# Performance work log

Hardware: AMD Instinct MI355X
Metric: run time of the kernel (lower is better)

Reference implementation:

```python
import jax, jax.numpy as jnp
import numpy as np

B, N, D = 1, 1024, 3584
H, KVH, HD = 28, 4, 128
I = 18944
SEC = [16, 24, 24]  # mrope_section, sums to HD//2
EPS_RMS = 1e-6
EPS_SM = 1e-6


def setup_inputs() -> dict:
    key = jax.random.key(0)
    ks = jax.random.split(key, 16)
    s = 0.02
    return {
        "hidden_states": jax.random.normal(ks[0], (B, N, D), jnp.float32),
        "cos": jax.random.uniform(ks[1], (3, B, N, HD), jnp.float32, -1.0, 1.0),
        "sin": jax.random.uniform(ks[2], (3, B, N, HD), jnp.float32, -1.0, 1.0),
        "prune_mask": jax.random.randint(ks[3], (B, N), 0, 2, jnp.int32),
        "Wq": jax.random.normal(ks[4], (D, H * HD), jnp.float32) * s,
        "bq": jnp.zeros((H * HD,), jnp.float32),
        "Wk": jax.random.normal(ks[5], (D, KVH * HD), jnp.float32) * s,
        "bk": jnp.zeros((KVH * HD,), jnp.float32),
        "Wv": jax.random.normal(ks[6], (D, KVH * HD), jnp.float32) * s,
        "bv": jnp.zeros((KVH * HD,), jnp.float32),
        "Wo": jax.random.normal(ks[7], (H * HD, D), jnp.float32) * s,
        "ln1_w": jnp.ones((D,), jnp.float32),
        "ln2_w": jnp.ones((D,), jnp.float32),
        "Wg": jax.random.normal(ks[8], (D, I), jnp.float32) * s,
        "Wu": jax.random.normal(ks[9], (D, I), jnp.float32) * s,
        "Wd": jax.random.normal(ks[10], (I, D), jnp.float32) * s,
    }


def _rmsnorm(x, w):
    v = jnp.mean(x * x, axis=-1, keepdims=True)
    return x * jax.lax.rsqrt(v + EPS_RMS) * w


def _rotate_half(x):
    h = x.shape[-1] // 2
    return jnp.concatenate([-x[..., h:], x[..., :h]], axis=-1)


def _mrope_select(t):
    # t: (3, B, N, HD) -> (B, 1, N, HD), picking section i from axis i%3
    parts, idx = [], 0
    for i, s in enumerate(SEC * 2):
        parts.append(t[i % 3, :, :, idx:idx + s])
        idx += s
    return jnp.concatenate(parts, axis=-1)[:, None]


def reference(hidden_states, cos, sin, prune_mask, Wq, bq, Wk, bk, Wv, bv, Wo,
              ln1_w, ln2_w, Wg, Wu, Wd):
    x = _rmsnorm(hidden_states, ln1_w)
    q = (x @ Wq + bq).reshape(B, N, H, HD).transpose(0, 2, 1, 3)
    k = (x @ Wk + bk).reshape(B, N, KVH, HD).transpose(0, 2, 1, 3)
    v = (x @ Wv + bv).reshape(B, N, KVH, HD).transpose(0, 2, 1, 3)

    cf, sf = _mrope_select(cos), _mrope_select(sin)
    q = q * cf + _rotate_half(q) * sf
    k = k * cf + _rotate_half(k) * sf

    groups = H // KVH
    k = jnp.repeat(k, groups, axis=1)  # (B,H,N,HD)
    v = jnp.repeat(v, groups, axis=1)

    scores = jnp.einsum("bhqd,bhkd->bhqk", q, k) / np.sqrt(HD).astype(np.float32)
    causal = jnp.tril(jnp.ones((N, N), bool))
    scores = jnp.where(causal, scores, jnp.float32(-1e9))

    # custom prune-masked softmax (softmax_with_mask)
    am = prune_mask.astype(jnp.float32)[:, None, None, :]  # (B,1,1,N)
    eye = jnp.eye(N, dtype=jnp.float32)
    am = am + (1.0 - am) * eye
    mx = jnp.max(scores, axis=-1, keepdims=True)
    e = jnp.exp(scores - mx) * am
    attn = (e + EPS_SM / N) / (jnp.sum(e, axis=-1, keepdims=True) + EPS_SM)

    o = jnp.einsum("bhqk,bhkd->bhqd", attn, v)
    o = o.transpose(0, 2, 1, 3).reshape(B, N, H * HD) @ Wo

    h = hidden_states + o
    y = _rmsnorm(h, ln2_w)
    mlp = (jax.nn.silu(y @ Wg) * (y @ Wu)) @ Wd
    return h + mlp
```

## Files before the change

kernel.cpp:

```cpp
#include <hip/hip_runtime.h>
#include <hip/hip_bf16.h>


#define SEQ   1024
#define DIM   3584
#define NH    28
#define NKVH  4
#define HDIM  128
#define IDIM  18944
#define QKVN  4608
#define GUN   37888

typedef __attribute__((ext_vector_type(8))) __bf16 bf16x8;
typedef __attribute__((ext_vector_type(4))) __bf16 bf16x4;
typedef __attribute__((ext_vector_type(4))) float  f32x4;

static constexpr size_t OFF_WQKVT = 0;
static constexpr size_t OFF_WOT   = OFF_WQKVT + (size_t)QKVN*DIM*2;
static constexpr size_t OFF_WGUT  = OFF_WOT   + (size_t)DIM*DIM*2;
static constexpr size_t OFF_WDT   = OFF_WGUT  + (size_t)GUN*DIM*2;
static constexpr size_t OFF_XB    = OFF_WDT   + (size_t)DIM*IDIM*2;
static constexpr size_t OFF_QKV   = OFF_XB    + (size_t)SEQ*DIM*2;
static constexpr size_t OFF_VT    = OFF_QKV   + (size_t)SEQ*QKVN*2;
static constexpr size_t OFF_VSUMP = OFF_VT    + (size_t)NKVH*HDIM*SEQ*2;
static constexpr size_t OFF_VSUM  = OFF_VSUMP + 4*8*128*4;
static constexpr size_t OFF_BQKV  = OFF_VSUM  + 4*128*4;
static constexpr size_t OFF_OB    = OFF_BQKV  + (size_t)QKVN*4;
static constexpr size_t OFF_HB    = OFF_OB    + (size_t)SEQ*DIM*2;
static constexpr size_t OFF_YB    = OFF_HB    + (size_t)SEQ*DIM*4;
static constexpr size_t OFF_GU    = OFF_YB    + (size_t)SEQ*DIM*2;
static constexpr size_t OFF_PB    = OFF_GU    + (size_t)SEQ*GUN*2;
static constexpr size_t OFF_PART  = OFF_GU;

#define GLL16(gp, lp)                                                        \
  __builtin_amdgcn_global_load_lds(                                         \
      (const __attribute__((address_space(1))) void*)(gp),                  \
      (__attribute__((address_space(3))) void*)(lp), 16, 0, 0)

#define BAR    asm volatile("s_barrier" ::: "memory")
#define LGKM0  asm volatile("s_waitcnt lgkmcnt(0)" ::: "memory")
#define VM4    asm volatile("s_waitcnt vmcnt(4)" ::: "memory")

__global__ __launch_bounds__(256) void transconv_kernel(
    const float* __restrict__ W, __bf16* __restrict__ WT, int K, int N, int mode)
{
  __shared__ __bf16 t[64][72];
  const int tid = threadIdx.x;
  const int k0 = blockIdx.y * 64, n0 = blockIdx.x * 64;
#pragma unroll
  for (int it = 0; it < 4; ++it) {
    int idx = it * 256 + tid;
    int r = idx >> 4, c4 = idx & 15;
    float4 v = *(const float4*)(W + (size_t)(k0 + r) * N + n0 + c4 * 4);
    t[r][c4 * 4 + 0] = (__bf16)v.x;
    t[r][c4 * 4 + 1] = (__bf16)v.y;
    t[r][c4 * 4 + 2] = (__bf16)v.z;
    t[r][c4 * 4 + 3] = (__bf16)v.w;
  }
  __syncthreads();
#pragma unroll
  for (int it = 0; it < 2; ++it) {
    int idx = it * 256 + tid;
    int r = idx >> 3, c8 = idx & 7;
    bf16x8 o;
#pragma unroll
    for (int i = 0; i < 8; ++i) o[i] = t[c8 * 8 + i][r];
    const int nlog = n0 + r;
    const int orow = (mode == 0) ? nlog
                   : ((nlog >> 4) << 5) + ((mode == 2) ? 16 : 0) + (nlog & 15);
    *(bf16x8*)(WT + (size_t)orow * K + k0 + c8 * 8) = o;
  }
}

__global__ __launch_bounds__(256) void pack_bias_kernel(
    const float* __restrict__ bq, const float* __restrict__ bk,
    const float* __restrict__ bv, float* __restrict__ out)
{
  int i = blockIdx.x * 256 + threadIdx.x;
  if (i < DIM) out[i] = bq[i];
  else if (i < DIM + 512) out[i] = bk[i - DIM];
  else if (i < QKVN) out[i] = bv[i - DIM - 512];
}

__global__ __launch_bounds__(256) void rmsnorm_kernel(
    const float* __restrict__ in, const float* __restrict__ w,
    __bf16* __restrict__ out)
{
  const int row = blockIdx.x;
  const int t = threadIdx.x;
  const float* x = in + (size_t)row * DIM;
  float4 v[4];
  float ss = 0.f;
#pragma unroll
  for (int i = 0; i < 4; ++i) {
    int idx = t + i * 256;
    if (idx < 896) {
      v[i] = ((const float4*)x)[idx];
      ss += v[i].x * v[i].x + v[i].y * v[i].y + v[i].z * v[i].z + v[i].w * v[i].w;
    }
  }
#pragma unroll
  for (int m = 1; m < 64; m <<= 1) ss += __shfl_xor(ss, m);
  __shared__ float red[4];
  if ((t & 63) == 0) red[t >> 6] = ss;
  __syncthreads();
  float tot = red[0] + red[1] + red[2] + red[3];
  float rs = rsqrtf(tot / (float)DIM + 1e-6f);
#pragma unroll
  for (int i = 0; i < 4; ++i) {
    int idx = t + i * 256;
    if (idx < 896) {
      float4 wv = ((const float4*)w)[idx];
      bf16x4 o;
      o[0] = (__bf16)(v[i].x * rs * wv.x);
      o[1] = (__bf16)(v[i].y * rs * wv.y);
      o[2] = (__bf16)(v[i].z * rs * wv.z);
      o[3] = (__bf16)(v[i].w * rs * wv.w);
      *(bf16x4*)(out + (size_t)row * DIM + idx * 4) = o;
    }
  }
}

template<int S, bool BF16OUT, bool BIAS>
__global__ __launch_bounds__(256) void reduce_kernel(
    const float* __restrict__ part, const float* __restrict__ resid,
    const float* __restrict__ bias, void* __restrict__ out, int N, int MN4)
{
  const int i4 = blockIdx.x * 256 + threadIdx.x;
  if (i4 >= MN4) return;
  const size_t base = (size_t)i4 * 4;
  f32x4 s = *(const f32x4*)(part + base);
#pragma unroll
  for (int k = 1; k < S; ++k)
    s += *(const f32x4*)(part + (size_t)k * MN4 * 4 + base);
  if (BIAS) {
    const int col = (int)(base % N);
    s += *(const f32x4*)(bias + col);
  }
  if (resid != nullptr) s += *(const f32x4*)(resid + base);
  if (BF16OUT) {
    bf16x4 o;
#pragma unroll
    for (int j = 0; j < 4; ++j) o[j] = (__bf16)s[j];
    *(bf16x4*)((__bf16*)out + base) = o;
  } else {
    *(f32x4*)((float*)out + base) = s;
  }
}

__global__ __launch_bounds__(256) void qkv_reduce_rope_kernel(
    const float* __restrict__ part, const float* __restrict__ bias,
    const float* __restrict__ cosb, const float* __restrict__ sinb,
    __bf16* __restrict__ qkv)
{
  const int n = blockIdx.x;
  const int t = threadIdx.x;
  const size_t rb = (size_t)n * QKVN;
  const size_t slab = (size_t)SEQ * QKVN;

  const int head = t >> 3;
  const int d0 = (t & 7) * 8;
  const int col = (head < NH) ? head * HDIM + d0 : DIM + (head - NH) * HDIM + d0;

  float lo[8], hi[8];
#pragma unroll
  for (int j = 0; j < 8; j += 4) {
    f32x4 a  = *(const f32x4*)(part + rb + col + j);
    f32x4 b  = *(const f32x4*)(part + slab + rb + col + j);
    f32x4 bi = *(const f32x4*)(bias + col + j);
    f32x4 a2  = *(const f32x4*)(part + rb + col + 64 + j);
    f32x4 b2  = *(const f32x4*)(part + slab + rb + col + 64 + j);
    f32x4 bi2 = *(const f32x4*)(bias + col + 64 + j);
#pragma unroll
    for (int i = 0; i < 4; ++i) {
      lo[j + i] = a[i] + b[i] + bi[i];
      hi[j + i] = a2[i] + b2[i] + bi2[i];
    }
  }
  bf16x8 olo, ohi;
#pragma unroll
  for (int j = 0; j < 8; ++j) {
    const int d = d0 + j;
    const int src = (d < 16) ? 0 : (d < 40) ? 1 : 2;
    const float* cb = cosb + ((size_t)src * SEQ + n) * HDIM;
    const float* sb = sinb + ((size_t)src * SEQ + n) * HDIM;
    const float c0 = cb[d], s0 = sb[d];
    const float c1 = cb[d + 64], s1 = sb[d + 64];
    olo[j] = (__bf16)(lo[j] * c0 - hi[j] * s0);
    ohi[j] = (__bf16)(hi[j] * c1 + lo[j] * s1);
  }
  *(bf16x8*)(qkv + rb + col) = olo;
  *(bf16x8*)(qkv + rb + col + 64) = ohi;

  {
    const int vc = 4096 + t * 2;
    float2 a  = *(const float2*)(part + rb + vc);
    float2 b  = *(const float2*)(part + slab + rb + vc);
    float2 bi = *(const float2*)(bias + vc);
    qkv[rb + vc]     = (__bf16)(a.x + b.x + bi.x);
    qkv[rb + vc + 1] = (__bf16)(a.y + b.y + bi.y);
  }
}

__global__ __launch_bounds__(256) void reduce_rms_kernel(
    const float* __restrict__ part, const float* __restrict__ resid,
    const float* __restrict__ w, float* __restrict__ hout,
    __bf16* __restrict__ yout)
{
  const int row = blockIdx.x;
  const int t = threadIdx.x;
  const size_t base = (size_t)row * DIM;
  const size_t slab = (size_t)SEQ * DIM;
  f32x4 v[4];
  float ss = 0.f;
#pragma unroll
  for (int i = 0; i < 4; ++i) {
    int idx = t + i * 256;
    if (idx < 896) {
      f32x4 s = *(const f32x4*)(part + base + idx * 4);
      s += *(const f32x4*)(part + slab + base + idx * 4);
      s += *(const f32x4*)(part + 2 * slab + base + idx * 4);
      s += *(const f32x4*)(part + 3 * slab + base + idx * 4);
      s += *(const f32x4*)(resid + base + idx * 4);
      v[i] = s;
      ss += s[0] * s[0] + s[1] * s[1] + s[2] * s[2] + s[3] * s[3];
      *(f32x4*)(hout + base + idx * 4) = s;
    }
  }
#pragma unroll
  for (int m = 1; m < 64; m <<= 1) ss += __shfl_xor(ss, m);
  __shared__ float red[4];
  if ((t & 63) == 0) red[t >> 6] = ss;
  __syncthreads();
  float tot = red[0] + red[1] + red[2] + red[3];
  float rs = rsqrtf(tot / (float)DIM + 1e-6f);
#pragma unroll
  for (int i = 0; i < 4; ++i) {
    int idx = t + i * 256;
    if (idx < 896) {
      f32x4 wv = *(const f32x4*)(w + idx * 4);
      bf16x4 o;
#pragma unroll
      for (int j = 0; j < 4; ++j) o[j] = (__bf16)(v[i][j] * rs * wv[j]);
      *(bf16x4*)(yout + base + idx * 4) = o;
    }
  }
}

template<int EPI>
__global__ __launch_bounds__(512, 1) void gemm256_kernel(
    const __bf16* __restrict__ A, const __bf16* __restrict__ BT,
    void* __restrict__ OUT, int M, int N, int K, int Kc, int gridY)
{
  __shared__ int4 lds4[8192];
  char* ldsc = (char*)lds4;
  const int tid = threadIdx.x;
  const int l = tid & 63, w = tid >> 6;
  const int wr = w >> 2, wc = w & 3;
  const int lg = l >> 4, lc = l & 15;

  const int nwg = gridDim.x;
  const int bq8 = nwg >> 3, br8 = nwg & 7;
  const int xcd = blockIdx.x & 7, bidx = blockIdx.x >> 3;
  const int wg = (xcd < br8 ? xcd * (bq8 + 1) : br8 * (bq8 + 1) + (xcd - br8) * bq8) + bidx;
  const int ntn = N >> 8;
  const int wg2 = wg / gridY;
  const int row0 = (wg % gridY) * 256;
  const int col0 = (wg2 % ntn) * 256;
  const int ks_ = wg2 / ntn;
  const int kbase = ks_ * Kc;

  size_t aoffj[2], boffj[2];
  int dstj[2];
#pragma unroll
  for (int j = 0; j < 2; ++j) {
    const int c = (j * 8 + w) * 64 + l;
    const int r = c >> 3, p = c & 7;
    const int b = p ^ (r & 7);
    aoffj[j] = (size_t)(row0 + r) * K + kbase + b * 8;
    boffj[j] = (size_t)(col0 + r) * K + kbase + b * 8;
    dstj[j] = (j * 8 + w) * 1024;
  }

#define STG_A(U, KT, BUFB) do {                                              \
    GLL16(A + aoffj[0] + (size_t)(U) * 128 * K + (size_t)(KT) * 64,          \
          ldsc + (BUFB) + (U) * 16384 + dstj[0]);                            \
    GLL16(A + aoffj[1] + (size_t)(U) * 128 * K + (size_t)(KT) * 64,          \
          ldsc + (BUFB) + (U) * 16384 + dstj[1]); } while (0)
#define STG_B(U, KT, BUFB) do {                                              \
    GLL16(BT + boffj[0] + (size_t)(U) * 128 * K + (size_t)(KT) * 64,         \
          ldsc + (BUFB) + 32768 + (U) * 16384 + dstj[0]);                    \
    GLL16(BT + boffj[1] + (size_t)(U) * 128 * K + (size_t)(KT) * 64,         \
          ldsc + (BUFB) + 32768 + (U) * 16384 + dstj[1]); } while (0)

  const int sw = lc & 7;
  const int rdA = (wr * 128 + lc) * 128;
  const int rdB = 32768 + (wc * 64 + lc) * 128;
  const int sk0 = (lg ^ sw) * 16;
  const int sk1 = ((4 | lg) ^ sw) * 16;

  f32x4 acc[8][4] = {};
  bf16x8 af[4][2], bfr[4][2];

#define RD_A4(MH, BUFB) do { _Pragma("unroll")                               \
    for (int mm = 0; mm < 4; ++mm) {                                         \
      af[mm][0] = *(const bf16x8*)(ldsc + (BUFB) + rdA + ((MH) * 4 + mm) * 2048 + sk0); \
      af[mm][1] = *(const bf16x8*)(ldsc + (BUFB) + rdA + ((MH) * 4 + mm) * 2048 + sk1); } } while (0)
#define RD_B2(NL, BUFB) do { _Pragma("unroll")                               \
    for (int nn = 0; nn < 2; ++nn) {                                         \
      bfr[(NL) + nn][0] = *(const bf16x8*)(ldsc + (BUFB) + rdB + ((NL) + nn) * 2048 + sk0); \
      bfr[(NL) + nn][1] = *(const bf16x8*)(ldsc + (BUFB) + rdB + ((NL) + nn) * 2048 + sk1); } } while (0)

#define MFMA16(MH, NL) do { _Pragma("unroll")                                \
    for (int mm = 0; mm < 4; ++mm) { _Pragma("unroll")                       \
      for (int nn = 0; nn < 2; ++nn) {                                       \
        acc[(MH)*4+mm][(NL)+nn] = __builtin_amdgcn_mfma_f32_16x16x32_bf16(   \
            af[mm][0], bfr[(NL)+nn][0], acc[(MH)*4+mm][(NL)+nn], 0, 0, 0);   \
        acc[(MH)*4+mm][(NL)+nn] = __builtin_amdgcn_mfma_f32_16x16x32_bf16(   \
            af[mm][1], bfr[(NL)+nn][1], acc[(MH)*4+mm][(NL)+nn], 0, 0, 0); } } } while (0)

#define DO_MFMA(MH, NL)                                                      \
    __builtin_amdgcn_s_setprio(1); MFMA16(MH, NL);                           \
    __builtin_amdgcn_s_setprio(0)

  STG_B(0, 0, 0); STG_B(1, 0, 0); STG_A(0, 0, 0); STG_A(1, 0, 0);
  STG_B(0, 1, 65536); STG_B(1, 1, 65536);
  VM4;
  BAR;
  RD_A4(0, 0); RD_B2(0, 0);

  const int T = Kc >> 6;
#pragma unroll 1
  for (int i = 0; i < (T >> 1); ++i) {
    const int t1 = 2 * i + 1;
    const int se = (2 * i + 2 < T) ? 2 * i + 2 : 2 * i;
    const int so = (2 * i + 3 < T) ? 2 * i + 3 : t1;
    LGKM0; DO_MFMA(0, 0); RD_B2(2, 0); STG_A(0, t1, 65536); BAR;
    LGKM0; DO_MFMA(0, 2); RD_A4(1, 0); STG_A(1, t1, 65536); BAR;
    LGKM0; DO_MFMA(1, 2); STG_B(0, se, 0); BAR;
    DO_MFMA(1, 0); STG_B(1, se, 0); VM4; RD_A4(0, 65536); RD_B2(0, 65536); BAR;
    LGKM0; DO_MFMA(0, 0); RD_B2(2, 65536); STG_A(0, se, 0); BAR;
    LGKM0; DO_MFMA(0, 2); RD_A4(1, 65536); STG_A(1, se, 0); BAR;
    LGKM0; DO_MFMA(1, 2); STG_B(0, so, 65536); BAR;
    DO_MFMA(1, 0); STG_B(1, so, 65536); VM4; RD_A4(0, 0); RD_B2(0, 0); BAR;
  }
  asm volatile("s_waitcnt vmcnt(0)" ::: "memory");
  LGKM0;

  if (EPI == 0) {
    __bf16* PBo = (__bf16*)OUT;
    const int id = N >> 1;
    const int baseq = (col0 + wc * 64) >> 5;
#pragma unroll
    for (int m = 0; m < 8; ++m) {
#pragma unroll
      for (int p = 0; p < 2; ++p) {
        const int gcol = (baseq + p) * 16 + lc;
#pragma unroll
        for (int j = 0; j < 4; ++j) {
          const int row = row0 + wr * 128 + m * 16 + lg * 4 + j;
          const float g = acc[m][2 * p][j];
          const float u = acc[m][2 * p + 1][j];
          const float s = g / (1.f + __expf(-g));
          PBo[(size_t)row * id + gcol] = (__bf16)(s * u);
        }
      }
    }
  } else {
    float* P = (float*)OUT + (size_t)ks_ * M * N;
#pragma unroll
    for (int m = 0; m < 8; ++m)
#pragma unroll
      for (int n = 0; n < 4; ++n)
#pragma unroll
        for (int j = 0; j < 4; ++j)
          P[(size_t)(row0 + wr * 128 + m * 16 + lg * 4 + j) * N
            + (col0 + wc * 64 + n * 16 + lc)] = acc[m][n][j];
  }
#undef STG_A
#undef STG_B
#undef RD_A4
#undef RD_B2
#undef MFMA16
#undef DO_MFMA
}

__global__ __launch_bounds__(256) void vtrans_kernel(
    const __bf16* __restrict__ qkv, __bf16* __restrict__ vT,
    float* __restrict__ vsump)
{
  __shared__ __bf16 t[128][132];
  const int nt = blockIdx.x, kvh = blockIdx.y;
  const int n0 = nt * 128;
  const int tid = threadIdx.x;
#pragma unroll
  for (int it = 0; it < 8; ++it) {
    int idx = it * 256 + tid;
    int nl = idx >> 4, c8 = idx & 15;
    bf16x8 v = *(const bf16x8*)(qkv + (size_t)(n0 + nl) * QKVN + 4096 + kvh * HDIM + c8 * 8);
#pragma unroll
    for (int i = 0; i < 8; ++i) t[nl][c8 * 8 + i] = v[i];
  }
  __syncthreads();
#pragma unroll
  for (int it = 0; it < 8; ++it) {
    int idx = it * 256 + tid;
    int d = idx >> 4, c8 = idx & 15;
    bf16x8 o;
#pragma unroll
    for (int i = 0; i < 8; ++i) o[i] = t[c8 * 8 + i][d];
    *(bf16x8*)(vT + (size_t)(kvh * HDIM + d) * SEQ + n0 + c8 * 8) = o;
  }
  if (tid < 128) {
    float s = 0.f;
    for (int nl = 0; nl < 128; ++nl) s += (float)t[nl][tid];
    vsump[(size_t)(kvh * 8 + nt) * 128 + tid] = s;
  }
}

__global__ __launch_bounds__(512) void vsum_reduce_kernel(
    const float* __restrict__ vsump, float* __restrict__ vsum)
{
  const int idx = threadIdx.x;
  const int kvh = idx >> 7, d = idx & 127;
  float s = 0.f;
#pragma unroll
  for (int nt = 0; nt < 8; ++nt) s += vsump[(size_t)(kvh * 8 + nt) * 128 + d];
  vsum[idx] = s;
}

__global__ __launch_bounds__(256) void attn_kernel(
    const __bf16* __restrict__ qkv, const __bf16* __restrict__ vT,
    const float* __restrict__ vsum, const int* __restrict__ prune,
    __bf16* __restrict__ o)
{
  __shared__ __bf16 plds[4 * 16 * 40];
  const int tid = threadIdx.x;
  const int l = tid & 63, w = tid >> 6;
  const int h = blockIdx.y;
  const int kvh = h / 7;
  const int qt = blockIdx.x;
  const int qbase = qt * 64 + w * 16;
  const int lg = l >> 4, lc = l & 15;
  __bf16* pw = plds + w * (16 * 40);

  bf16x8 qf[4];
#pragma unroll
  for (int s = 0; s < 4; ++s)
    qf[s] = *(const bf16x8*)(qkv + (size_t)(qbase + lc) * QKVN + h * HDIM + s * 32 + lg * 8);

  f32x4 oacc[8] = {};
  float mrun[4] = {-3e38f, -3e38f, -3e38f, -3e38f};
  float lrun[4] = {0.f, 0.f, 0.f, 0.f};

  const int kbEnd = ((qbase + 15) >> 5) + 1;
  for (int kb = 0; kb < kbEnd; ++kb) {
    f32x4 sacc[2] = {};
#pragma unroll
    for (int s = 0; s < 4; ++s) {
#pragma unroll
      for (int c = 0; c < 2; ++c) {
        bf16x8 kf = *(const bf16x8*)(qkv + (size_t)(kb * 32 + c * 16 + lc) * QKVN
                                     + DIM + kvh * HDIM + s * 32 + lg * 8);
        sacc[c] = __builtin_amdgcn_mfma_f32_16x16x32_bf16(qf[s], kf, sacc[c], 0, 0, 0);
      }
    }
    float p[2][4];
    int am[2];
#pragma unroll
    for (int c = 0; c < 2; ++c) {
      const int col = kb * 32 + c * 16 + lc;
      am[c] = (prune[col] != 0) ? 1 : 0;
#pragma unroll
      for (int j = 0; j < 4; ++j) {
        const int row = qbase + lg * 4 + j;
        float sv = sacc[c][j] * 0.08838834764831845f;
        p[c][j] = (col <= row) ? sv : -3e38f;
      }
    }
#pragma unroll
    for (int j = 0; j < 4; ++j) {
      float mx = fmaxf(p[0][j], p[1][j]);
      mx = fmaxf(mx, __shfl_xor(mx, 1));
      mx = fmaxf(mx, __shfl_xor(mx, 2));
      mx = fmaxf(mx, __shfl_xor(mx, 4));
      mx = fmaxf(mx, __shfl_xor(mx, 8));
      const float mnew = fmaxf(mrun[j], mx);
      const float scale = __expf(mrun[j] - mnew);
      mrun[j] = mnew;
      const int row = qbase + lg * 4 + j;
      float rs = 0.f;
#pragma unroll
      for (int c = 0; c < 2; ++c) {
        const int col = kb * 32 + c * 16 + lc;
        float e = __expf(p[c][j] - mnew);
        const int keep = (col == row) ? 1 : am[c];
        e = keep ? e : 0.f;
        p[c][j] = e;
        rs += e;
      }
      rs += __shfl_xor(rs, 1);
      rs += __shfl_xor(rs, 2);
      rs += __shfl_xor(rs, 4);
      rs += __shfl_xor(rs, 8);
      lrun[j] = lrun[j] * scale + rs;
#pragma unroll
      for (int df = 0; df < 8; ++df) oacc[df][j] *= scale;
    }
#pragma unroll
    for (int c = 0; c < 2; ++c)
#pragma unroll
      for (int j = 0; j < 4; ++j)
        pw[(lg * 4 + j) * 40 + c * 16 + lc] = (__bf16)p[c][j];
    bf16x8 pa = *(const bf16x8*)(pw + lc * 40 + lg * 8);
#pragma unroll
    for (int df = 0; df < 8; ++df) {
      bf16x8 vf = *(const bf16x8*)(vT + (size_t)(kvh * HDIM + df * 16 + lc) * SEQ + kb * 32 + lg * 8);
      oacc[df] = __builtin_amdgcn_mfma_f32_16x16x32_bf16(pa, vf, oacc[df], 0, 0, 0);
    }
  }
#pragma unroll
  for (int df = 0; df < 8; ++df) {
    const float vs = vsum[kvh * HDIM + df * 16 + lc];
#pragma unroll
    for (int j = 0; j < 4; ++j) {
      const int row = qbase + lg * 4 + j;
      const float denom = lrun[j] + 1e-6f;
      const float val = (oacc[df][j] + 9.765625e-10f * vs) / denom;
      o[(size_t)row * DIM + h * HDIM + df * 16 + lc] = (__bf16)val;
    }
  }
}

extern "C" void kernel_launch(void* const* d_in, const int* in_sizes, int n_in,
                              void* d_out, int out_size, void* d_ws, size_t ws_size,
                              hipStream_t stream) {
  const float* hidden = (const float*)d_in[0];
  const float* cosb   = (const float*)d_in[1];
  const float* sinb   = (const float*)d_in[2];
  const int*   prune  = (const int*)d_in[3];
  const float* Wq     = (const float*)d_in[4];
  const float* bq     = (const float*)d_in[5];
  const float* Wk     = (const float*)d_in[6];
  const float* bk     = (const float*)d_in[7];
  const float* Wv     = (const float*)d_in[8];
  const float* bv     = (const float*)d_in[9];
  const float* Wo     = (const float*)d_in[10];
  const float* ln1    = (const float*)d_in[11];
  const float* ln2    = (const float*)d_in[12];
  const float* Wg     = (const float*)d_in[13];
  const float* Wu     = (const float*)d_in[14];
  const float* Wd     = (const float*)d_in[15];
  float* out = (float*)d_out;
  char* ws = (char*)d_ws;

  __bf16* WQKVT = (__bf16*)(ws + OFF_WQKVT);
  __bf16* WOT   = (__bf16*)(ws + OFF_WOT);
  __bf16* WGUT  = (__bf16*)(ws + OFF_WGUT);
  __bf16* WDT   = (__bf16*)(ws + OFF_WDT);
  __bf16* XB    = (__bf16*)(ws + OFF_XB);
  __bf16* QKV   = (__bf16*)(ws + OFF_QKV);
  __bf16* VT    = (__bf16*)(ws + OFF_VT);
  float*  VSUMP = (float*)(ws + OFF_VSUMP);
  float*  VSUM  = (float*)(ws + OFF_VSUM);
  float*  BQKV  = (float*)(ws + OFF_BQKV);
  __bf16* OB    = (__bf16*)(ws + OFF_OB);
  float*  HB    = (float*)(ws + OFF_HB);
  __bf16* YB    = (__bf16*)(ws + OFF_YB);
  __bf16* PB    = (__bf16*)(ws + OFF_PB);
  float*  PART  = (float*)(ws + OFF_PART);

  transconv_kernel<<<dim3(DIM / 64, DIM / 64), 256, 0, stream>>>(Wq, WQKVT, DIM, DIM, 0);
  transconv_kernel<<<dim3(512 / 64, DIM / 64), 256, 0, stream>>>(Wk, WQKVT + (size_t)DIM * DIM, DIM, 512, 0);
  transconv_kernel<<<dim3(512 / 64, DIM / 64), 256, 0, stream>>>(Wv, WQKVT + (size_t)4096 * DIM, DIM, 512, 0);
  pack_bias_kernel<<<QKVN / 256, 256, 0, stream>>>(bq, bk, bv, BQKV);
  rmsnorm_kernel<<<SEQ, 256, 0, stream>>>(hidden, ln1, XB);

  gemm256_kernel<1><<<(SEQ / 256) * (QKVN / 256) * 2, 512, 0, stream>>>(
      XB, WQKVT, PART, SEQ, QKVN, DIM, DIM / 2, SEQ / 256);
  qkv_reduce_rope_kernel<<<SEQ, 256, 0, stream>>>(PART, BQKV, cosb, sinb, QKV);

  vtrans_kernel<<<dim3(8, NKVH), 256, 0, stream>>>(QKV, VT, VSUMP);
  vsum_reduce_kernel<<<1, 512, 0, stream>>>(VSUMP, VSUM);
  attn_kernel<<<dim3(SEQ / 64, NH), 256, 0, stream>>>(QKV, VT, VSUM, prune, OB);

  transconv_kernel<<<dim3(DIM / 64, DIM / 64), 256, 0, stream>>>(Wo, WOT, DIM, DIM, 0);
  gemm256_kernel<1><<<(DIM / 256) * (SEQ / 256) * 4, 512, 0, stream>>>(
      OB, WOT, PART, SEQ, DIM, DIM, DIM / 4, SEQ / 256);
  reduce_rms_kernel<<<SEQ, 256, 0, stream>>>(PART, hidden, ln2, HB, YB);

  transconv_kernel<<<dim3(IDIM / 64, DIM / 64), 256, 0, stream>>>(Wg, WGUT, DIM, IDIM, 1);
  transconv_kernel<<<dim3(IDIM / 64, DIM / 64), 256, 0, stream>>>(Wu, WGUT, DIM, IDIM, 2);
  gemm256_kernel<0><<<(GUN / 256) * (SEQ / 256), 512, 0, stream>>>(
      YB, WGUT, PB, SEQ, GUN, DIM, DIM, SEQ / 256);

  transconv_kernel<<<dim3(DIM / 64, IDIM / 64), 256, 0, stream>>>(Wd, WDT, IDIM, DIM, 0);
  gemm256_kernel<1><<<(DIM / 256) * (SEQ / 256) * 4, 512, 0, stream>>>(
      PB, WDT, PART, SEQ, DIM, IDIM, IDIM / 4, SEQ / 256);
  reduce_kernel<4, false, false><<<(SEQ * DIM / 4 + 255) / 256, 256, 0, stream>>>(
      PART, HB, nullptr, out, DIM, SEQ * DIM / 4);
}
```

Before: 910.0 us.

## Fuse fp32 weight transpose-convert into GEMM B-tile loading for Wo/Wg/Wu/Wd

Removes the separate transpose-and-convert-to-bf16 passes for the Wo, Wg/Wu and Wd weights. The GEMM now reads the fp32 row-major weights directly into registers, converts them to bf16 and writes them swizzled into LDS, with the gate/up interleave handled in the address math. This avoids writing and re-reading roughly 200MB of intermediate bf16 weights. In exchange the B loads become strided scalar fp32 reads at double the byte count, issued through registers instead of async global-to-LDS copies, which can stall the MFMA pipeline.

```diff
diff --git a/kernel.cpp b/kernel.cpp
--- a/kernel.cpp
+++ b/kernel.cpp
@@ -16,10 +16,7 @@
 typedef __attribute__((ext_vector_type(4))) float  f32x4;
 
 static constexpr size_t OFF_WQKVT = 0;
-static constexpr size_t OFF_WOT   = OFF_WQKVT + (size_t)QKVN*DIM*2;
-static constexpr size_t OFF_WGUT  = OFF_WOT   + (size_t)DIM*DIM*2;
-static constexpr size_t OFF_WDT   = OFF_WGUT  + (size_t)GUN*DIM*2;
-static constexpr size_t OFF_XB    = OFF_WDT   + (size_t)DIM*IDIM*2;
+static constexpr size_t OFF_XB    = OFF_WQKVT + (size_t)QKVN*DIM*2;
 static constexpr size_t OFF_QKV   = OFF_XB    + (size_t)SEQ*DIM*2;
 static constexpr size_t OFF_VT    = OFF_QKV   + (size_t)SEQ*QKVN*2;
 static constexpr size_t OFF_VSUMP = OFF_VT    + (size_t)NKVH*HDIM*SEQ*2;
@@ -40,9 +37,12 @@
 #define BAR    asm volatile("s_barrier" ::: "memory")
 #define LGKM0  asm volatile("s_waitcnt lgkmcnt(0)" ::: "memory")
 #define VM4    asm volatile("s_waitcnt vmcnt(4)" ::: "memory")
+#define VM18   asm volatile("s_waitcnt vmcnt(18)" ::: "memory")
+#define VM0    asm volatile("s_waitcnt vmcnt(0)" ::: "memory")
+#define LGKM12 asm volatile("s_waitcnt lgkmcnt(12)" ::: "memory")
 
 __global__ __launch_bounds__(256) void transconv_kernel(
-    const float* __restrict__ W, __bf16* __restrict__ WT, int K, int N, int mode)
+    const float* __restrict__ W, __bf16* __restrict__ WT, int K, int N)
 {
   __shared__ __bf16 t[64][72];
   const int tid = threadIdx.x;
@@ -65,10 +65,7 @@
     bf16x8 o;
 #pragma unroll
     for (int i = 0; i < 8; ++i) o[i] = t[c8 * 8 + i][r];
-    const int nlog = n0 + r;
-    const int orow = (mode == 0) ? nlog
-                   : ((nlog >> 4) << 5) + ((mode == 2) ? 16 : 0) + (nlog & 15);
-    *(bf16x8*)(WT + (size_t)orow * K + k0 + c8 * 8) = o;
+    *(bf16x8*)(WT + (size_t)(n0 + r) * K + k0 + c8 * 8) = o;
   }
 }
 
@@ -247,9 +244,10 @@
   }
 }
 
-template<int EPI>
+template<int EPI, int BSRC, int LDB>
 __global__ __launch_bounds__(512, 1) void gemm256_kernel(
     const __bf16* __restrict__ A, const __bf16* __restrict__ BT,
+    const float* __restrict__ Bg, const float* __restrict__ Bu,
     void* __restrict__ OUT, int M, int N, int K, int Kc, int gridY)
 {
   __shared__ int4 lds4[8192];
@@ -270,16 +268,36 @@
   const int ks_ = wg2 / ntn;
   const int kbase = ks_ * Kc;
 
-  size_t aoffj[2], boffj[2];
+  size_t aoffj[2];
   int dstj[2];
+  size_t boffj[2];
 #pragma unroll
   for (int j = 0; j < 2; ++j) {
     const int c = (j * 8 + w) * 64 + l;
     const int r = c >> 3, p = c & 7;
     const int b = p ^ (r & 7);
     aoffj[j] = (size_t)(row0 + r) * K + kbase + b * 8;
-    boffj[j] = (size_t)(col0 + r) * K + kbase + b * 8;
+    if (BSRC == 0) boffj[j] = (size_t)(col0 + r) * K + kbase + b * 8;
     dstj[j] = (j * 8 + w) * 1024;
+  }
+
+  const int lb16 = l & 15;
+  const int lbk = (l >> 4) * 16;
+  const float* srcB0 = nullptr;
+  const float* srcB1 = nullptr;
+  if (BSRC != 0) {
+#pragma unroll
+    for (int U = 0; U < 2; ++U) {
+      const int np = col0 + U * 128 + w * 16 + lb16;
+      const float* s;
+      if (BSRC == 2) {
+        const int nlog = ((np >> 5) << 4) + (np & 15);
+        s = (((np >> 4) & 1) ? Bu : Bg) + nlog;
+      } else {
+        s = Bg + np;
+      }
+      if (U == 0) srcB0 = s; else srcB1 = s;
+    }
   }
 
 #define STG_A(U, KT, BUFB) do {                                              \
@@ -293,6 +311,22 @@
     GLL16(BT + boffj[1] + (size_t)(U) * 128 * K + (size_t)(KT) * 64,         \
           ldsc + (BUFB) + 32768 + (U) * 16384 + dstj[1]); } while (0)
 
+#define BL(arr, KT, U) do {                                                  \
+    const float* _p = ((U) ? srcB1 : srcB0)                                  \
+                      + (size_t)(kbase + (KT) * 64 + lbk) * (size_t)LDB;     \
+    _Pragma("unroll") for (int _j = 0; _j < 16; ++_j)                        \
+      arr[_j] = _p[(size_t)_j * (size_t)LDB]; } while (0)
+#define BW(arr, BUFB, U) do {                                                \
+    const int _pr = (U) * 128 + w * 16 + lb16;                               \
+    char* _wp = ldsc + (BUFB) + 32768 + _pr * 128;                           \
+    const int _sw = _pr & 7;                                                 \
+    const int _c0 = (l >> 4) * 2;                                            \
+    bf16x8 _v0, _v1;                                                         \
+    _Pragma("unroll") for (int _j = 0; _j < 8; ++_j) {                       \
+      _v0[_j] = (__bf16)arr[_j]; _v1[_j] = (__bf16)arr[8 + _j]; }            \
+    *(bf16x8*)(_wp + ((_c0 ^ _sw) * 16)) = _v0;                              \
+    *(bf16x8*)(_wp + (((_c0 + 1) ^ _sw) * 16)) = _v1; } while (0)
+
   const int sw = lc & 7;
   const int rdA = (wr * 128 + lc) * 128;
   const int rdB = 32768 + (wc * 64 + lc) * 128;
@@ -323,28 +357,56 @@
     __builtin_amdgcn_s_setprio(1); MFMA16(MH, NL);                           \
     __builtin_amdgcn_s_setprio(0)
 
-  STG_B(0, 0, 0); STG_B(1, 0, 0); STG_A(0, 0, 0); STG_A(1, 0, 0);
-  STG_B(0, 1, 65536); STG_B(1, 1, 65536);
-  VM4;
-  BAR;
-  RD_A4(0, 0); RD_B2(0, 0);
-
   const int T = Kc >> 6;
+
+  if (BSRC == 0) {
+    STG_B(0, 0, 0); STG_B(1, 0, 0); STG_A(0, 0, 0); STG_A(1, 0, 0);
+    STG_B(0, 1, 65536); STG_B(1, 1, 65536);
+    VM4;
+    BAR;
+    RD_A4(0, 0); RD_B2(0, 0);
 #pragma unroll 1
-  for (int i = 0; i < (T >> 1); ++i) {
-    const int t1 = 2 * i + 1;
-    const int se = (2 * i + 2 < T) ? 2 * i + 2 : 2 * i;
-    const int so = (2 * i + 3 < T) ? 2 * i + 3 : t1;
-    LGKM0; DO_MFMA(0, 0); RD_B2(2, 0); STG_A(0, t1, 65536); BAR;
-    LGKM0; DO_MFMA(0, 2); RD_A4(1, 0); STG_A(1, t1, 65536); BAR;
-    LGKM0; DO_MFMA(1, 2); STG_B(0, se, 0); BAR;
-    DO_MFMA(1, 0); STG_B(1, se, 0); VM4; RD_A4(0, 65536); RD_B2(0, 65536); BAR;
-    LGKM0; DO_MFMA(0, 0); RD_B2(2, 65536); STG_A(0, se, 0); BAR;
-    LGKM0; DO_MFMA(0, 2); RD_A4(1, 65536); STG_A(1, se, 0); BAR;
-    LGKM0; DO_MFMA(1, 2); STG_B(0, so, 65536); BAR;
-    DO_MFMA(1, 0); STG_B(1, so, 65536); VM4; RD_A4(0, 0); RD_B2(0, 0); BAR;
-  }
-  asm volatile("s_waitcnt vmcnt(0)" ::: "memory");
+    for (int i = 0; i < (T >> 1); ++i) {
+      const int t1 = 2 * i + 1;
+      const int se = (2 * i + 2 < T) ? 2 * i + 2 : 2 * i;
+      const int so = (2 * i + 3 < T) ? 2 * i + 3 : t1;
+      LGKM0; DO_MFMA(0, 0); RD_B2(2, 0); STG_A(0, t1, 65536); BAR;
+      LGKM0; DO_MFMA(0, 2); RD_A4(1, 0); STG_A(1, t1, 65536); BAR;
+      LGKM0; DO_MFMA(1, 2); STG_B(0, se, 0); BAR;
+      DO_MFMA(1, 0); STG_B(1, se, 0); VM4; RD_A4(0, 65536); RD_B2(0, 65536); BAR;
+      LGKM0; DO_MFMA(0, 0); RD_B2(2, 65536); STG_A(0, se, 0); BAR;
+      LGKM0; DO_MFMA(0, 2); RD_A4(1, 65536); STG_A(1, se, 0); BAR;
+      LGKM0; DO_MFMA(1, 2); STG_B(0, so, 65536); BAR;
+      DO_MFMA(1, 0); STG_B(1, so, 65536); VM4; RD_A4(0, 0); RD_B2(0, 0); BAR;
+    }
+  } else {
+    float blA[16], blB[16];
+    STG_A(0, 0, 0); STG_A(1, 0, 0);
+    BL(blA, 0, 0); BL(blB, 0, 1);
+    VM0;
+    BW(blA, 0, 0); BW(blB, 0, 1);
+    BL(blA, 1, 0); BL(blB, 1, 1);
+    VM0;
+    BW(blA, 65536, 0); BW(blB, 65536, 1);
+    LGKM0;
+    BAR;
+    RD_A4(0, 0); RD_B2(0, 0);
+#pragma unroll 1
+    for (int i = 0; i < (T >> 1); ++i) {
+      const int t1 = 2 * i + 1;
+      const int se = (2 * i + 2 < T) ? 2 * i + 2 : 2 * i;
+      const int so = (2 * i + 3 < T) ? 2 * i + 3 : t1;
+      LGKM0; DO_MFMA(0, 0); RD_B2(2, 0); STG_A(0, t1, 65536); BL(blA, se, 0); BAR;
+      LGKM0; DO_MFMA(0, 2); RD_A4(1, 0); STG_A(1, t1, 65536); BL(blB, se, 1); BAR;
+      LGKM0; DO_MFMA(1, 2); VM18; BW(blA, 0, 0); LGKM0; BAR;
+      DO_MFMA(1, 0); VM0; BW(blB, 0, 1); RD_A4(0, 65536); RD_B2(0, 65536); LGKM12; BAR;
+      LGKM0; DO_MFMA(0, 0); RD_B2(2, 65536); STG_A(0, se, 0); BL(blA, so, 0); BAR;
+      LGKM0; DO_MFMA(0, 2); RD_A4(1, 65536); STG_A(1, se, 0); BL(blB, so, 1); BAR;
+      LGKM0; DO_MFMA(1, 2); VM18; BW(blA, 65536, 0); LGKM0; BAR;
+      DO_MFMA(1, 0); VM0; BW(blB, 65536, 1); RD_A4(0, 0); RD_B2(0, 0); LGKM12; BAR;
+    }
+  }
+  VM0;
   LGKM0;
 
   if (EPI == 0) {
@@ -379,6 +441,8 @@
   }
 #undef STG_A
 #undef STG_B
+#undef BL
+#undef BW
 #undef RD_A4
 #undef RD_B2
 #undef MFMA16
@@ -555,9 +619,6 @@
   char* ws = (char*)d_ws;
 
   __bf16* WQKVT = (__bf16*)(ws + OFF_WQKVT);
-  __bf16* WOT   = (__bf16*)(ws + OFF_WOT);
-  __bf16* WGUT  = (__bf16*)(ws + OFF_WGUT);
-  __bf16* WDT   = (__bf16*)(ws + OFF_WDT);
   __bf16* XB    = (__bf16*)(ws + OFF_XB);
   __bf16* QKV   = (__bf16*)(ws + OFF_QKV);
   __bf16* VT    = (__bf16*)(ws + OFF_VT);
@@ -570,33 +631,29 @@
   __bf16* PB    = (__bf16*)(ws + OFF_PB);
   float*  PART  = (float*)(ws + OFF_PART);
 
-  transconv_kernel<<<dim3(DIM / 64, DIM / 64), 256, 0, stream>>>(Wq, WQKVT, DIM, DIM, 0);
-  transconv_kernel<<<dim3(512 / 64, DIM / 64), 256, 0, stream>>>(Wk, WQKVT + (size_t)DIM * DIM, DIM, 512, 0);
-  transconv_kernel<<<dim3(512 / 64, DIM / 64), 256, 0, stream>>>(Wv, WQKVT + (size_t)4096 * DIM, DIM, 512, 0);
+  transconv_kernel<<<dim3(DIM / 64, DIM / 64), 256, 0, stream>>>(Wq, WQKVT, DIM, DIM);
+  transconv_kernel<<<dim3(512 / 64, DIM / 64), 256, 0, stream>>>(Wk, WQKVT + (size_t)DIM * DIM, DIM, 512);
+  transconv_kernel<<<dim3(512 / 64, DIM / 64), 256, 0, stream>>>(Wv, WQKVT + (size_t)4096 * DIM, DIM, 512);
   pack_bias_kernel<<<QKVN / 256, 256, 0, stream>>>(bq, bk, bv, BQKV);
   rmsnorm_kernel<<<SEQ, 256, 0, stream>>>(hidden, ln1, XB);
 
-  gemm256_kernel<1><<<(SEQ / 256) * (QKVN / 256) * 2, 512, 0, stream>>>(
-      XB, WQKVT, PART, SEQ, QKVN, DIM, DIM / 2, SEQ / 256);
+  gemm256_kernel<1, 0, 0><<<(SEQ / 256) * (QKVN / 256) * 2, 512, 0, stream>>>(
+      XB, WQKVT, nullptr, nullptr, PART, SEQ, QKVN, DIM, DIM / 2, SEQ / 256);
   qkv_reduce_rope_kernel<<<SEQ, 256, 0, stream>>>(PART, BQKV, cosb, sinb, QKV);
 
   vtrans_kernel<<<dim3(8, NKVH), 256, 0, stream>>>(QKV, VT, VSUMP);
   vsum_reduce_kernel<<<1, 512, 0, stream>>>(VSUMP, VSUM);
   attn_kernel<<<dim3(SEQ / 64, NH), 256, 0, stream>>>(QKV, VT, VSUM, prune, OB);
 
-  transconv_kernel<<<dim3(DIM / 64, DIM / 64), 256, 0, stream>>>(Wo, WOT, DIM, DIM, 0);
-  gemm256_kernel<1><<<(DIM / 256) * (SEQ / 256) * 4, 512, 0, stream>>>(
-      OB, WOT, PART, SEQ, DIM, DIM, DIM / 4, SEQ / 256);
+  gemm256_kernel<1, 1, DIM><<<(DIM / 256) * (SEQ / 256) * 4, 512, 0, stream>>>(
+      OB, nullptr, Wo, nullptr, PART, SEQ, DIM, DIM, DIM / 4, SEQ / 256);
   reduce_rms_kernel<<<SEQ, 256, 0, stream>>>(PART, hidden, ln2, HB, YB);
 
-  transconv_kernel<<<dim3(IDIM / 64, DIM / 64), 256, 0, stream>>>(Wg, WGUT, DIM, IDIM, 1);
-  transconv_kernel<<<dim3(IDIM / 64, DIM / 64), 256, 0, stream>>>(Wu, WGUT, DIM, IDIM, 2);
-  gemm256_kernel<0><<<(GUN / 256) * (SEQ / 256), 512, 0, stream>>>(
-      YB, WGUT, PB, SEQ, GUN, DIM, DIM, SEQ / 256);
-
-  transconv_kernel<<<dim3(DIM / 64, IDIM / 64), 256, 0, stream>>>(Wd, WDT, IDIM, DIM, 0);
-  gemm256_kernel<1><<<(DIM / 256) * (SEQ / 256) * 4, 512, 0, stream>>>(
-      PB, WDT, PART, SEQ, DIM, IDIM, IDIM / 4, SEQ / 256);
+  gemm256_kernel<0, 2, IDIM><<<(GUN / 256) * (SEQ / 256), 512, 0, stream>>>(
+      YB, nullptr, Wg, Wu, PB, SEQ, GUN, DIM, DIM, SEQ / 256);
+
+  gemm256_kernel<1, 1, DIM><<<(DIM / 256) * (SEQ / 256) * 4, 512, 0, stream>>>(
+      PB, nullptr, Wd, nullptr, PART, SEQ, DIM, IDIM, IDIM / 4, SEQ / 256);
   reduce_kernel<4, false, false><<<(SEQ * DIM / 4 + 255) / 256, 256, 0, stream>>>(
       PART, HB, nullptr, out, DIM, SEQ * DIM / 4);
 }
```

Measured after the change: 1.193 ms. +31.1%, slower.
